# Kernel optimization log

Measured on AMD Instinct MI355X. Metric: run time of the kernel, lower is better.

Reference implementation:

```python
import jax, jax.numpy as jnp
import numpy as np

BIG = 1000000.0
EPS = 1e-06
COST_CLASS, COST_BBOX, COST_GIOU = 1.0, 5.0, 2.0


def sanitize_boxes(boxes):
    # boxes: [..., 4] cxcywh
    boxes = jnp.nan_to_num(boxes, nan=0.0, posinf=1.0, neginf=0.0)
    cx, cy, w, h = jnp.moveaxis(boxes, -1, 0)
    cx = jnp.clip(cx, 0.0, 1.0)
    cy = jnp.clip(cy, 0.0, 1.0)
    w = jnp.clip(w, EPS, 1.0)
    h = jnp.clip(h, EPS, 1.0)
    return jnp.stack([cx, cy, w, h], axis=-1)


def box_cxcywh_to_xyxy(x):
    cx, cy, w, h = jnp.moveaxis(x, -1, 0)
    return jnp.stack([cx - 0.5 * w, cy - 0.5 * h, cx + 0.5 * w, cy + 0.5 * h], axis=-1)


def pairwise_giou(b1, b2):
    # b1: [B, Q, 4] xyxy, b2: [B, T, 4] xyxy -> [B, Q, T]
    area1 = (b1[..., 2] - b1[..., 0]) * (b1[..., 3] - b1[..., 1])  # [B,Q]
    area2 = (b2[..., 2] - b2[..., 0]) * (b2[..., 3] - b2[..., 1])  # [B,T]
    lt = jnp.maximum(b1[:, :, None, :2], b2[:, None, :, :2])  # [B,Q,T,2]
    rb = jnp.minimum(b1[:, :, None, 2:], b2[:, None, :, 2:])
    wh = jnp.clip(rb - lt, 0.0)
    inter = wh[..., 0] * wh[..., 1]  # [B,Q,T]
    union = area1[:, :, None] + area2[:, None, :] - inter
    iou = inter / union
    # enclosing box
    lt_c = jnp.minimum(b1[:, :, None, :2], b2[:, None, :, :2])
    rb_c = jnp.maximum(b1[:, :, None, 2:], b2[:, None, :, 2:])
    wh_c = jnp.clip(rb_c - lt_c, 0.0)
    area_c = wh_c[..., 0] * wh_c[..., 1]
    return iou - (area_c - union) / area_c


def reference(pred_logits, pred_boxes, tgt_labels, tgt_boxes):
    # Batched cost-matrix construction of HungarianMatcher.forward.
    out_logits = jnp.nan_to_num(pred_logits, nan=0.0, posinf=0.0, neginf=0.0)
    out_prob = jax.nn.softmax(out_logits, axis=-1)  # [B,Q,C]
    out_bbox = sanitize_boxes(pred_boxes)           # [B,Q,4]
    t_bbox = sanitize_boxes(tgt_boxes)              # [B,T,4]

    # cost_class[b,q,t] = -out_prob[b,q,tgt_labels[b,t]]
    B, Q, C = out_prob.shape
    T = tgt_labels.shape[1]
    gather_idx = jnp.broadcast_to(tgt_labels[:, None, :], (B, Q, T))
    cost_class = -jnp.take_along_axis(out_prob, gather_idx, axis=2)  # [B,Q,T]

    # L1 cdist in cxcywh space
    cost_bbox = jnp.sum(jnp.abs(out_bbox[:, :, None, :] - t_bbox[:, None, :, :]), axis=-1)

    cost_giou = -pairwise_giou(box_cxcywh_to_xyxy(out_bbox), box_cxcywh_to_xyxy(t_bbox))

    Cmat = COST_CLASS * cost_class + COST_BBOX * cost_bbox + COST_GIOU * cost_giou
    return jnp.nan_to_num(Cmat, nan=BIG, posinf=BIG, neginf=BIG)


def setup_inputs() -> dict:
    key = jax.random.key(0)
    k1, k2, k3, k4 = jax.random.split(key, 4)
    B, Q, C, T = 64, 900, 256, 200
    return {
        "pred_logits": jax.random.normal(k1, (B, Q, C), dtype=jnp.float32),
        "pred_boxes": jax.random.uniform(k2, (B, Q, 4), dtype=jnp.float32),
        "tgt_labels": jax.random.randint(k3, (B, T), 0, C),
        "tgt_boxes": jax.random.uniform(k4, (B, T, 4), dtype=jnp.float32),
    }
```

## Files before the change

### kernel.cpp

```cpp
#include <hip/hip_runtime.h>
#include <math.h>

constexpr int B = 64, Q = 900, C = 256, T = 200;
constexpr float EPSV = 1e-6f;
constexpr int WPB = 4;
constexpr int QPW = 8;
constexpr int QPB = WPB * QPW;

__device__ __forceinline__ float clampf(float x, float lo, float hi) {
    return fminf(fmaxf(x, lo), hi);
}

__global__ __launch_bounds__(256, 6)
void matcher_kernel(const float* __restrict__ logits,
                    const float* __restrict__ pboxes,
                    const int*   __restrict__ tlabels,
                    const float* __restrict__ tboxes,
                    float* __restrict__ out)
{
    __shared__ float s_exp[WPB][C][2];

    const int blocks_per_b = (Q + QPB - 1) / QPB;
    const int b    = blockIdx.x / blocks_per_b;
    const int qblk = blockIdx.x % blocks_per_b;
    const int wave = threadIdx.x >> 6;
    const int lane = threadIdx.x & 63;
    const int q0   = qblk * QPB + wave * QPW;
    if (q0 >= Q) return;

    float tx0[4], ty0[4], tx1[4], ty1[4], tw[4], th[4];
    int   lidx[4];
    const float* tb_base = tboxes + b * (T * 4);
    const int*   tl_base = tlabels + b * T;
    #pragma unroll
    for (int s = 0; s < 4; ++s) {
        int t  = lane + 64 * s;
        int tc = t < T ? t : T - 1;
        float4 tb = ((const float4*)tb_base)[tc];
        float cx = clampf(tb.x, 0.0f, 1.0f);
        float cy = clampf(tb.y, 0.0f, 1.0f);
        float w  = clampf(tb.z, EPSV, 1.0f);
        float h  = clampf(tb.w, EPSV, 1.0f);
        tw[s] = w;  th[s] = h;
        tx0[s] = cx - 0.5f * w;  ty0[s] = cy - 0.5f * h;
        tx1[s] = cx + 0.5f * w;  ty1[s] = cy + 0.5f * h;
        int lab = tl_base[tc];
        lidx[s] = min(max(lab, 0), C - 1);
    }

    const unsigned rowa0 = (unsigned)b * Q + q0;

    #pragma unroll
    for (int i = 0; i < 4; ++i) {
        const unsigned rowa = rowa0 + i;
        const bool vb = (q0 + i + 4) < Q;
        const unsigned rowb = vb ? rowa + 4 : rowa;

        const float4 lga = ((const float4*)(logits + (size_t)rowa * C))[lane];
        const float4 lgb = ((const float4*)(logits + (size_t)rowb * C))[lane];
        const float4 pba = *(const float4*)(pboxes + (size_t)rowa * 4);
        const float4 pbb = *(const float4*)(pboxes + (size_t)rowb * 4);

        float ea0 = __expf(lga.x), ea1 = __expf(lga.y);
        float ea2 = __expf(lga.z), ea3 = __expf(lga.w);
        float eb0 = __expf(lgb.x), eb1 = __expf(lgb.y);
        float eb2 = __expf(lgb.z), eb3 = __expf(lgb.w);
        float sa = (ea0 + ea1) + (ea2 + ea3);
        float sb = (eb0 + eb1) + (eb2 + eb3);
        #pragma unroll
        for (int off = 32; off; off >>= 1) {
            sa += __shfl_xor(sa, off);
            sb += __shfl_xor(sb, off);
        }
        const float inva = __builtin_amdgcn_rcpf(sa);
        const float invb = __builtin_amdgcn_rcpf(sb);

        float* dst = &s_exp[wave][4 * lane][0];
        ((float4*)dst)[0] = make_float4(ea0, eb0, ea1, eb1);
        ((float4*)dst)[1] = make_float4(ea2, eb2, ea3, eb3);

        float pcxa = clampf(pba.x, 0.0f, 1.0f), pcya = clampf(pba.y, 0.0f, 1.0f);
        float pwa  = clampf(pba.z, EPSV, 1.0f), pha  = clampf(pba.w, EPSV, 1.0f);
        float pax0 = pcxa - 0.5f * pwa, pay0 = pcya - 0.5f * pha;
        float pax1 = pcxa + 0.5f * pwa, pay1 = pcya + 0.5f * pha;
        float psxa = pax0 + pax1, psya = pay0 + pay1;
        float pareaa = pwa * pha;

        float pcxb = clampf(pbb.x, 0.0f, 1.0f), pcyb = clampf(pbb.y, 0.0f, 1.0f);
        float pwb  = clampf(pbb.z, EPSV, 1.0f), phb  = clampf(pbb.w, EPSV, 1.0f);
        float pbx0 = pcxb - 0.5f * pwb, pby0 = pcyb - 0.5f * phb;
        float pbx1 = pcxb + 0.5f * pwb, pby1 = pcyb + 0.5f * phb;
        float psxb = pbx0 + pbx1, psyb = pby0 + pby1;
        float pareab = pwb * phb;

        float* orowa = out + (size_t)rowa * T;
        float* orowb = out + (size_t)rowb * T;

        #pragma unroll
        for (int s = 0; s < 4; ++s) {
            const float* g2 = &s_exp[wave][lidx[s]][0];
            float ga = g2[0], gb = g2[1];
            float tsx = tx0[s] + tx1[s];
            float tsy = ty0[s] + ty1[s];
            float tarea = tw[s] * th[s];

            {
                float t0 = fmaf(-ga, inva, 2.0f);
                float s1 = fabsf(psxa - tsx) + fabsf(psya - tsy);
                float s2 = fabsf(pwa - tw[s]) + fabsf(pha - th[s]);
                float iw = fmaxf(fminf(pax1, tx1[s]) - fmaxf(pax0, tx0[s]), 0.0f);
                float ih = fmaxf(fminf(pay1, ty1[s]) - fmaxf(pay0, ty0[s]), 0.0f);
                float inter = iw * ih;
                float uni = pareaa + tarea - inter;
                float cw = fmaxf(pax1, tx1[s]) - fminf(pax0, tx0[s]);
                float ch = fmaxf(pay1, ty1[s]) - fminf(pay0, ty0[s]);
                float ca = cw * ch;
                float num = fmaf(uni, uni, inter * ca);
                float val = num * __builtin_amdgcn_rcpf(uni * ca);
                float cost = fmaf(2.5f, s1, t0);
                cost = fmaf(5.0f, s2, cost);
                cost = fmaf(-2.0f, val, cost);
                int t = lane + 64 * s;
                if (t < T) orowa[t] = cost;
            }
            if (vb) {
                float t0 = fmaf(-gb, invb, 2.0f);
                float s1 = fabsf(psxb - tsx) + fabsf(psyb - tsy);
                float s2 = fabsf(pwb - tw[s]) + fabsf(phb - th[s]);
                float iw = fmaxf(fminf(pbx1, tx1[s]) - fmaxf(pbx0, tx0[s]), 0.0f);
                float ih = fmaxf(fminf(pby1, ty1[s]) - fmaxf(pby0, ty0[s]), 0.0f);
                float inter = iw * ih;
                float uni = pareab + tarea - inter;
                float cw = fmaxf(pbx1, tx1[s]) - fminf(pbx0, tx0[s]);
                float ch = fmaxf(pby1, ty1[s]) - fminf(pby0, ty0[s]);
                float ca = cw * ch;
                float num = fmaf(uni, uni, inter * ca);
                float val = num * __builtin_amdgcn_rcpf(uni * ca);
                float cost = fmaf(2.5f, s1, t0);
                cost = fmaf(5.0f, s2, cost);
                cost = fmaf(-2.0f, val, cost);
                int t = lane + 64 * s;
                if (t < T) orowb[t] = cost;
            }
        }
    }
}

extern "C" void kernel_launch(void* const* d_in, const int* in_sizes, int n_in,
                              void* d_out, int out_size, void* d_ws, size_t ws_size,
                              hipStream_t stream) {
    const float* logits  = (const float*)d_in[0];
    const float* pboxes  = (const float*)d_in[1];
    const int*   tlabels = (const int*)d_in[2];
    const float* tboxes  = (const float*)d_in[3];
    float* out = (float*)d_out;

    const int blocks_per_b = (Q + QPB - 1) / QPB;
    dim3 grid(B * blocks_per_b);
    dim3 block(64 * WPB);
    matcher_kernel<<<grid, block, 0, stream>>>(logits, pboxes, tlabels, tboxes, out);
}
```

Measured before the change: 133.5 us.

## Give each lane four contiguous targets and store results as float4

Each lane now owns four consecutive targets (50 active lanes per wave), so each output row is written with one float4 store per lane instead of four strided scalar stores. Each wave now handles two queries instead of eight, the inner query loop is removed, and the grid grows fourfold with an occupancy hint of 8. The aim is wider, better-coalesced output writes, which dominate traffic, plus more parallelism for latency hiding. In exchange 14 lanes per wave sit idle in the compute phase, and the per-target setup runs for every pair of queries instead of every eight.

```diff
diff --git a/kernel.cpp b/kernel.cpp
--- a/kernel.cpp
+++ b/kernel.cpp
@@ -4,14 +4,15 @@
 constexpr int B = 64, Q = 900, C = 256, T = 200;
 constexpr float EPSV = 1e-6f;
 constexpr int WPB = 4;
-constexpr int QPW = 8;
+constexpr int QPW = 2;
 constexpr int QPB = WPB * QPW;
+constexpr int NT4 = T / 4;
 
 __device__ __forceinline__ float clampf(float x, float lo, float hi) {
     return fminf(fmaxf(x, lo), hi);
 }
 
-__global__ __launch_bounds__(256, 6)
+__global__ __launch_bounds__(256, 8)
 void matcher_kernel(const float* __restrict__ logits,
                     const float* __restrict__ pboxes,
                     const int*   __restrict__ tlabels,
@@ -28,121 +29,118 @@
     const int q0   = qblk * QPB + wave * QPW;
     if (q0 >= Q) return;
 
-    float tx0[4], ty0[4], tx1[4], ty1[4], tw[4], th[4];
+    const bool act = lane < NT4;
+    float tx0[4], ty0[4], tx1[4], ty1[4], twd[4], tht[4];
     int   lidx[4];
-    const float* tb_base = tboxes + b * (T * 4);
-    const int*   tl_base = tlabels + b * T;
+    {
+        const float* tb_base = tboxes + b * (T * 4);
+        const int*   tl_base = tlabels + b * T;
+        const int t0i = act ? 4 * lane : 0;
+        #pragma unroll
+        for (int s = 0; s < 4; ++s) {
+            int t = t0i + s;
+            float4 tb = ((const float4*)tb_base)[t];
+            float cx = clampf(tb.x, 0.0f, 1.0f);
+            float cy = clampf(tb.y, 0.0f, 1.0f);
+            float w  = clampf(tb.z, EPSV, 1.0f);
+            float h  = clampf(tb.w, EPSV, 1.0f);
+            twd[s] = w;  tht[s] = h;
+            tx0[s] = cx - 0.5f * w;  ty0[s] = cy - 0.5f * h;
+            tx1[s] = cx + 0.5f * w;  ty1[s] = cy + 0.5f * h;
+            lidx[s] = min(max(tl_base[t], 0), C - 1);
+        }
+    }
+
+    const size_t rowa = (size_t)b * Q + q0;
+    const size_t rowb = rowa + 1;
+
+    const float4 lga = ((const float4*)(logits + rowa * C))[lane];
+    const float4 lgb = ((const float4*)(logits + rowb * C))[lane];
+    const float4 pba = *(const float4*)(pboxes + rowa * 4);
+    const float4 pbb = *(const float4*)(pboxes + rowb * 4);
+
+    float ea0 = __expf(lga.x), ea1 = __expf(lga.y);
+    float ea2 = __expf(lga.z), ea3 = __expf(lga.w);
+    float eb0 = __expf(lgb.x), eb1 = __expf(lgb.y);
+    float eb2 = __expf(lgb.z), eb3 = __expf(lgb.w);
+    float sa = (ea0 + ea1) + (ea2 + ea3);
+    float sb = (eb0 + eb1) + (eb2 + eb3);
+    #pragma unroll
+    for (int off = 32; off; off >>= 1) {
+        sa += __shfl_xor(sa, off);
+        sb += __shfl_xor(sb, off);
+    }
+    const float inva = __builtin_amdgcn_rcpf(sa);
+    const float invb = __builtin_amdgcn_rcpf(sb);
+
+    float* dst = &s_exp[wave][4 * lane][0];
+    ((float4*)dst)[0] = make_float4(ea0, eb0, ea1, eb1);
+    ((float4*)dst)[1] = make_float4(ea2, eb2, ea3, eb3);
+
+    float pcxa = clampf(pba.x, 0.0f, 1.0f), pcya = clampf(pba.y, 0.0f, 1.0f);
+    float pwa  = clampf(pba.z, EPSV, 1.0f), pha  = clampf(pba.w, EPSV, 1.0f);
+    float pax0 = pcxa - 0.5f * pwa, pay0 = pcya - 0.5f * pha;
+    float pax1 = pcxa + 0.5f * pwa, pay1 = pcya + 0.5f * pha;
+    float psxa = pax0 + pax1, psya = pay0 + pay1;
+    float pareaa = pwa * pha;
+
+    float pcxb = clampf(pbb.x, 0.0f, 1.0f), pcyb = clampf(pbb.y, 0.0f, 1.0f);
+    float pwb  = clampf(pbb.z, EPSV, 1.0f), phb  = clampf(pbb.w, EPSV, 1.0f);
+    float pbx0 = pcxb - 0.5f * pwb, pby0 = pcyb - 0.5f * phb;
+    float pbx1 = pcxb + 0.5f * pwb, pby1 = pcyb + 0.5f * phb;
+    float psxb = pbx0 + pbx1, psyb = pby0 + pby1;
+    float pareab = pwb * phb;
+
+    float resa[4], resb[4];
     #pragma unroll
     for (int s = 0; s < 4; ++s) {
-        int t  = lane + 64 * s;
-        int tc = t < T ? t : T - 1;
-        float4 tb = ((const float4*)tb_base)[tc];
-        float cx = clampf(tb.x, 0.0f, 1.0f);
-        float cy = clampf(tb.y, 0.0f, 1.0f);
-        float w  = clampf(tb.z, EPSV, 1.0f);
-        float h  = clampf(tb.w, EPSV, 1.0f);
-        tw[s] = w;  th[s] = h;
-        tx0[s] = cx - 0.5f * w;  ty0[s] = cy - 0.5f * h;
-        tx1[s] = cx + 0.5f * w;  ty1[s] = cy + 0.5f * h;
-        int lab = tl_base[tc];
-        lidx[s] = min(max(lab, 0), C - 1);
+        const float* g2 = &s_exp[wave][lidx[s]][0];
+        const float ga = g2[0], gb = g2[1];
+        const float tsx = tx0[s] + tx1[s];
+        const float tsy = ty0[s] + ty1[s];
+        const float tarea = twd[s] * tht[s];
+
+        {
+            float t0 = fmaf(-ga, inva, 2.0f);
+            float s1 = fabsf(psxa - tsx) + fabsf(psya - tsy);
+            float s2 = fabsf(pwa - twd[s]) + fabsf(pha - tht[s]);
+            float iw = fmaxf(fminf(pax1, tx1[s]) - fmaxf(pax0, tx0[s]), 0.0f);
+            float ih = fmaxf(fminf(pay1, ty1[s]) - fmaxf(pay0, ty0[s]), 0.0f);
+            float inter = iw * ih;
+            float uni = pareaa + tarea - inter;
+            float cw = fmaxf(pax1, tx1[s]) - fminf(pax0, tx0[s]);
+            float ch = fmaxf(pay1, ty1[s]) - fminf(pay0, ty0[s]);
+            float ca = cw * ch;
+            float num = fmaf(uni, uni, inter * ca);
+            float val = num * __builtin_amdgcn_rcpf(uni * ca);
+            float cost = fmaf(2.5f, s1, t0);
+            cost = fmaf(5.0f, s2, cost);
+            resa[s] = fmaf(-2.0f, val, cost);
+        }
+        {
+            float t0 = fmaf(-gb, invb, 2.0f);
+            float s1 = fabsf(psxb - tsx) + fabsf(psyb - tsy);
+            float s2 = fabsf(pwb - twd[s]) + fabsf(phb - tht[s]);
+            float iw = fmaxf(fminf(pbx1, tx1[s]) - fmaxf(pbx0, tx0[s]), 0.0f);
+            float ih = fmaxf(fminf(pby1, ty1[s]) - fmaxf(pby0, ty0[s]), 0.0f);
+            float inter = iw * ih;
+            float uni = pareab + tarea - inter;
+            float cw = fmaxf(pbx1, tx1[s]) - fminf(pbx0, tx0[s]);
+            float ch = fmaxf(pby1, ty1[s]) - fminf(pby0, ty0[s]);
+            float ca = cw * ch;
+            float num = fmaf(uni, uni, inter * ca);
+            float val = num * __builtin_amdgcn_rcpf(uni * ca);
+            float cost = fmaf(2.5f, s1, t0);
+            cost = fmaf(5.0f, s2, cost);
+            resb[s] = fmaf(-2.0f, val, cost);
+        }
     }
 
-    const unsigned rowa0 = (unsigned)b * Q + q0;
-
-    #pragma unroll
-    for (int i = 0; i < 4; ++i) {
-        const unsigned rowa = rowa0 + i;
-        const bool vb = (q0 + i + 4) < Q;
-        const unsigned rowb = vb ? rowa + 4 : rowa;
-
-        const float4 lga = ((const float4*)(logits + (size_t)rowa * C))[lane];
-        const float4 lgb = ((const float4*)(logits + (size_t)rowb * C))[lane];
-        const float4 pba = *(const float4*)(pboxes + (size_t)rowa * 4);
-        const float4 pbb = *(const float4*)(pboxes + (size_t)rowb * 4);
-
-        float ea0 = __expf(lga.x), ea1 = __expf(lga.y);
-        float ea2 = __expf(lga.z), ea3 = __expf(lga.w);
-        float eb0 = __expf(lgb.x), eb1 = __expf(lgb.y);
-        float eb2 = __expf(lgb.z), eb3 = __expf(lgb.w);
-        float sa = (ea0 + ea1) + (ea2 + ea3);
-        float sb = (eb0 + eb1) + (eb2 + eb3);
-        #pragma unroll
-        for (int off = 32; off; off >>= 1) {
-            sa += __shfl_xor(sa, off);
-            sb += __shfl_xor(sb, off);
-        }
-        const float inva = __builtin_amdgcn_rcpf(sa);
-        const float invb = __builtin_amdgcn_rcpf(sb);
-
-        float* dst = &s_exp[wave][4 * lane][0];
-        ((float4*)dst)[0] = make_float4(ea0, eb0, ea1, eb1);
-        ((float4*)dst)[1] = make_float4(ea2, eb2, ea3, eb3);
-
-        float pcxa = clampf(pba.x, 0.0f, 1.0f), pcya = clampf(pba.y, 0.0f, 1.0f);
-        float pwa  = clampf(pba.z, EPSV, 1.0f), pha  = clampf(pba.w, EPSV, 1.0f);
-        float pax0 = pcxa - 0.5f * pwa, pay0 = pcya - 0.5f * pha;
-        float pax1 = pcxa + 0.5f * pwa, pay1 = pcya + 0.5f * pha;
-        float psxa = pax0 + pax1, psya = pay0 + pay1;
-        float pareaa = pwa * pha;
-
-        float pcxb = clampf(pbb.x, 0.0f, 1.0f), pcyb = clampf(pbb.y, 0.0f, 1.0f);
-        float pwb  = clampf(pbb.z, EPSV, 1.0f), phb  = clampf(pbb.w, EPSV, 1.0f);
-        float pbx0 = pcxb - 0.5f * pwb, pby0 = pcyb - 0.5f * phb;
-        float pbx1 = pcxb + 0.5f * pwb, pby1 = pcyb + 0.5f * phb;
-        float psxb = pbx0 + pbx1, psyb = pby0 + pby1;
-        float pareab = pwb * phb;
-
-        float* orowa = out + (size_t)rowa * T;
-        float* orowb = out + (size_t)rowb * T;
-
-        #pragma unroll
-        for (int s = 0; s < 4; ++s) {
-            const float* g2 = &s_exp[wave][lidx[s]][0];
-            float ga = g2[0], gb = g2[1];
-            float tsx = tx0[s] + tx1[s];
-            float tsy = ty0[s] + ty1[s];
-            float tarea = tw[s] * th[s];
-
-            {
-                float t0 = fmaf(-ga, inva, 2.0f);
-                float s1 = fabsf(psxa - tsx) + fabsf(psya - tsy);
-                float s2 = fabsf(pwa - tw[s]) + fabsf(pha - th[s]);
-                float iw = fmaxf(fminf(pax1, tx1[s]) - fmaxf(pax0, tx0[s]), 0.0f);
-                float ih = fmaxf(fminf(pay1, ty1[s]) - fmaxf(pay0, ty0[s]), 0.0f);
-                float inter = iw * ih;
-                float uni = pareaa + tarea - inter;
-                float cw = fmaxf(pax1, tx1[s]) - fminf(pax0, tx0[s]);
-                float ch = fmaxf(pay1, ty1[s]) - fminf(pay0, ty0[s]);
-                float ca = cw * ch;
-                float num = fmaf(uni, uni, inter * ca);
-                float val = num * __builtin_amdgcn_rcpf(uni * ca);
-                float cost = fmaf(2.5f, s1, t0);
-                cost = fmaf(5.0f, s2, cost);
-                cost = fmaf(-2.0f, val, cost);
-                int t = lane + 64 * s;
-                if (t < T) orowa[t] = cost;
-            }
-            if (vb) {
-                float t0 = fmaf(-gb, invb, 2.0f);
-                float s1 = fabsf(psxb - tsx) + fabsf(psyb - tsy);
-                float s2 = fabsf(pwb - tw[s]) + fabsf(phb - th[s]);
-                float iw = fmaxf(fminf(pbx1, tx1[s]) - fmaxf(pbx0, tx0[s]), 0.0f);
-                float ih = fmaxf(fminf(pby1, ty1[s]) - fmaxf(pby0, ty0[s]), 0.0f);
-                float inter = iw * ih;
-                float uni = pareab + tarea - inter;
-                float cw = fmaxf(pbx1, tx1[s]) - fminf(pbx0, tx0[s]);
-                float ch = fmaxf(pby1, ty1[s]) - fminf(pby0, ty0[s]);
-                float ca = cw * ch;
-                float num = fmaf(uni, uni, inter * ca);
-                float val = num * __builtin_amdgcn_rcpf(uni * ca);
-                float cost = fmaf(2.5f, s1, t0);
-                cost = fmaf(5.0f, s2, cost);
-                cost = fmaf(-2.0f, val, cost);
-                int t = lane + 64 * s;
-                if (t < T) orowb[t] = cost;
-            }
-        }
+    if (act) {
+        float4* oa = (float4*)(out + rowa * T);
+        float4* ob = (float4*)(out + rowb * T);
+        oa[lane] = make_float4(resa[0], resa[1], resa[2], resa[3]);
+        ob[lane] = make_float4(resb[0], resb[1], resb[2], resb[3]);
     }
 }
 
```

Result: faster. 113.4 us (-15.0%).
